# Performance work log

Hardware: AMD Instinct MI355X
Metric: run time of the kernel (lower is better)

## Reference

```python
import jax, jax.numpy as jnp
import numpy as np

EPS = 1e-5  # BatchNorm eps (eval mode, running_mean=0, running_var=1)

def bn(z, gamma, beta):
    s = gamma / jnp.sqrt(1.0 + EPS)
    return z * s[None, :, None, None] + beta[None, :, None, None]

def conv1d(x, w, b, pad):
    # x: (N,C,L), w: (O,C,K)
    y = jax.lax.conv_general_dilated(x, w, (1,), [(pad, pad)],
                                     dimension_numbers=('NCH', 'OIH', 'NCH'))
    return y + b[None, :, None]

def setup_inputs():
    key = jax.random.key(0)
    N, C, T, V = 128, 64, 128, 25
    S, H = 3, 8
    ig = C // 4   # gcn q/k embedding channels
    ih = C // H   # per-head channels
    ks = iter(jax.random.split(key, 40))
    rn = lambda shape, s=0.05: jax.random.normal(next(ks), shape, jnp.float32) * s
    inp = {}
    inp['x'] = jax.random.normal(next(ks), (N, C, T, V), jnp.float32)
    inp['A'] = jnp.stack([jnp.eye(V, dtype=jnp.float32)] * S) + jax.random.uniform(next(ks), (S, V, V), jnp.float32) * 0.05
    inp['alpha'] = jnp.float32(0.1)
    inp['Wq'] = rn((S, ig, C)); inp['bq'] = rn((S, ig))
    inp['Wk'] = rn((S, ig, C)); inp['bk'] = rn((S, ig))
    inp['Wf'] = rn((S, C, C)); inp['bf'] = rn((S, C))
    inp['g_gamma'] = jnp.ones((C,), jnp.float32); inp['g_beta'] = jnp.zeros((C,), jnp.float32)
    inp['W_sa'] = rn((1, C, V)); inp['b_sa'] = rn((1,))
    inp['W_ta'] = rn((1, C, 9)); inp['b_ta'] = rn((1,))
    inp['W_fc1'] = rn((C // 2, C)); inp['b_fc1'] = rn((C // 2,))
    inp['W_fc2'] = rn((C, C // 2)); inp['b_fc2'] = rn((C,))
    inp['pos_emb'] = rn((1, T, C * V), 0.02)
    inp['Wq_h'] = rn((H, ih, C)); inp['bq_h'] = rn((H, ih))
    inp['Wk_h'] = rn((H, ih, C)); inp['bk_h'] = rn((H, ih))
    inp['Wv_h'] = rn((H, ih, C)); inp['bv_h'] = rn((H, ih))
    inp['W_ffn'] = rn((C, C)); inp['b_ffn'] = rn((C,))
    inp['m_gamma'] = jnp.ones((C,), jnp.float32); inp['m_beta'] = jnp.zeros((C,), jnp.float32)
    return inp

def reference(x, A, alpha, Wq, bq, Wk, bk, Wf, bf, g_gamma, g_beta,
              W_sa, b_sa, W_ta, b_ta, W_fc1, b_fc1, W_fc2, b_fc2,
              pos_emb, Wq_h, bq_h, Wk_h, bk_h, Wv_h, bv_h,
              W_ffn, b_ffn, m_gamma, m_beta):
    N, C, T, V = x.shape
    S, ig = Wq.shape[0], Wq.shape[1]
    # ---------- unit_gcn_qkv (adaptive graph conv) ----------
    q = jnp.einsum('sic,nctv->nsitv', Wq, x) + bq[None, :, :, None, None]
    k = jnp.einsum('sic,nctv->nsitv', Wk, x) + bk[None, :, :, None, None]
    qf = q.transpose(0, 1, 4, 2, 3).reshape(N, S, V, ig * T)   # (N,S,V,ig*T)
    kf = k.reshape(N, S, ig * T, V)                            # (N,S,ig*T,V)
    att = jnp.einsum('nsvd,nsdw->nsvw', qf, kf) / jnp.float32(ig * T)
    att = jax.nn.softmax(att, axis=-2)                         # Softmax(dim=-2)
    Aad = A[None] + att * alpha                                # (N,S,V,V)
    xf = x.reshape(N, C * T, V)
    agg = jnp.einsum('ndv,nsvw->nsdw', xf, Aad).reshape(N, S, C, T, V)
    y = jnp.einsum('soc,nsctv->notv', Wf, agg) + bf.sum(0)[None, :, None, None]
    y = bn(y, g_gamma, g_beta) + x                             # down = identity (in==out)
    y = jax.nn.relu(y)
    # spatial / temporal / channel attention gates (MS-AAGCN style)
    se = y.mean(axis=2)                                        # (N,C,V)
    sa = jax.nn.sigmoid(conv1d(se, W_sa, b_sa, (V - 1) // 2))  # (N,1,V)
    y = y * sa[:, :, None, :] + y
    se = y.mean(axis=3)                                        # (N,C,T)
    ta = jax.nn.sigmoid(conv1d(se, W_ta, b_ta, 4))             # (N,1,T)
    y = y * ta[:, :, :, None] + y
    se = y.mean(axis=(2, 3))                                   # (N,C)
    ca = jax.nn.sigmoid(jax.nn.relu(se @ W_fc1.T + b_fc1) @ W_fc2.T + b_fc2)
    y = y * ca[:, :, None, None] + y
    # ---------- Multi-Head causal Temporal Attention ----------
    pe = pos_emb.reshape(1, T, C, V).transpose(0, 2, 1, 3)     # 'n t (d v)' -> 'n d t v'
    xa = y + pe
    H, ih = Wq_h.shape[0], Wq_h.shape[1]
    d = ih * V
    qh = (jnp.einsum('hoc,nctv->nhtov', Wq_h, xa) + bq_h[None, :, None, :, None]).reshape(N, H, T, d)
    kh = (jnp.einsum('hoc,nctv->nhtov', Wk_h, xa) + bk_h[None, :, None, :, None]).reshape(N, H, T, d)
    vh = (jnp.einsum('hoc,nctv->nhtov', Wv_h, xa) + bv_h[None, :, None, :, None]).reshape(N, H, T, d)
    scores = jnp.einsum('nhtd,nhsd->nhts', qh, kh) / jnp.sqrt(jnp.float32(d))
    causal = jnp.tril(jnp.ones((T, T), bool))
    scores = jnp.where(causal[None, None], scores, jnp.float32(-1e9))
    p = jax.nn.softmax(scores, axis=-1)
    oh = jnp.einsum('nhts,nhsd->nhtd', p, vh)
    # concat heads along emb dim, reinterpret '(d v)' -> channels-major layout
    z = oh.reshape(N, H, T, ih, V).transpose(0, 1, 3, 2, 4).reshape(N, C, T, V)
    z = bn(z, m_gamma, m_beta) + xa
    z = jax.nn.relu(jnp.einsum('oc,nctv->notv', W_ffn, z) + b_ffn[None, :, None, None]) + xa
    z = bn(z, m_gamma, m_beta)
    # ---------- unit residual ----------
    return jax.nn.relu(z + x)
```

## Files before the change

### kernel.cpp

```cpp
#include <hip/hip_runtime.h>
#include <hip/hip_bf16.h>

#define N_ 128
#define C_ 64
#define T_ 128
#define V_ 25
#define S_ 3
#define IG 16
#define IH 8
#define H_ 8
#define D_ 200
#define CV 1600
#define TV 3200
#define EPSB 1e-5f
#define NCHUNK 16

typedef __attribute__((ext_vector_type(8))) short short8v;
typedef __attribute__((ext_vector_type(4))) float f32x4;
#define MFMA16 __builtin_amdgcn_mfma_f32_16x16x32_bf16
#define ZIDX(r,c) ((r)*72 + ((c) ^ ((((r)>>3)&7)<<3)))

__device__ __forceinline__ float sigm(float x){ return 1.f/(1.f+expf(-x)); }
__device__ __forceinline__ float b2f(__hip_bfloat16 b){ return __bfloat162float(b); }
__device__ __forceinline__ __hip_bfloat16 f2b(float f){ return __float2bfloat16(f); }
__device__ __forceinline__ float ubl(unsigned int u){ return __uint_as_float(u<<16); }
__device__ __forceinline__ float ubh(unsigned int u){ return __uint_as_float(u & 0xffff0000u); }
__device__ __forceinline__ float sh2f(short s){ return __uint_as_float(((unsigned int)(unsigned short)s)<<16); }
__device__ __forceinline__ unsigned short f2bu(float f){
  unsigned int u = __float_as_uint(f);
  u += 0x7fff + ((u>>16)&1);
  return (unsigned short)(u>>16);
}
__device__ __forceinline__ unsigned long long pk4bf(f32x4 v){
  unsigned long long a = f2bu(v[0]);
  unsigned long long b = f2bu(v[1]);
  unsigned long long c = f2bu(v[2]);
  unsigned long long d = f2bu(v[3]);
  return a | (b<<16) | (c<<32) | (d<<48);
}

__global__ __launch_bounds__(256) void k_prep(
    const float* __restrict__ Wq, const float* __restrict__ Wk,
    const float* __restrict__ Wf,
    const float* __restrict__ Wq_h, const float* __restrict__ Wk_h,
    const float* __restrict__ Wv_h, const float* __restrict__ W_ffn,
    short* __restrict__ wqb, short* __restrict__ wkb, short* __restrict__ Wfb,
    short* __restrict__ w3b, short* __restrict__ Wffnb)
{
  const int i = blockIdx.x*256 + threadIdx.x;
  if (i < 3072){ wqb[i]=(short)f2bu(Wq[i]); wkb[i]=(short)f2bu(Wk[i]); }
  if (i < 12288) Wfb[i]=(short)f2bu(Wf[i]);
  if (i < 4096){
    w3b[i]      =(short)f2bu(Wq_h[i]);
    w3b[4096+i] =(short)f2bu(Wk_h[i]);
    w3b[8192+i] =(short)f2bu(Wv_h[i]);
    Wffnb[i]    =(short)f2bu(W_ffn[i]);
  }
}

__global__ __launch_bounds__(256) void k_gcn_att1(
    const float* __restrict__ x,
    const short* __restrict__ wqb, const float* __restrict__ bq,
    const short* __restrict__ wkb, const float* __restrict__ bk,
    float* __restrict__ attg)
{
  const int tc = blockIdx.x, n = blockIdx.y;
  const int tid = threadIdx.x;
  const int wv = tid>>6, l = tid&63, lc = l&15, lk = l>>4;
  __shared__ __align__(16) short xtb[4*32*72];
  __shared__ __align__(16) char QB[3*32*256];
  __shared__ __align__(16) char KB[3*32*256];
  __shared__ float bql[48], bkl[48];
  short8v aqf[3][2], akf[3][2];
  #pragma unroll
  for (int s=0;s<3;++s){
    #pragma unroll
    for (int ks=0;ks<2;++ks){
      aqf[s][ks] = *(const short8v*)(wqb + (s*16+lc)*64 + ks*32 + lk*8);
      akf[s][ks] = *(const short8v*)(wkb + (s*16+lc)*64 + ks*32 + lk*8);
    }
  }
  if (tid<48){ bql[tid]=bq[tid]; bkl[tid]=bk[tid]; }
  for (int i=tid;i<4*7*72;i+=256){
    int tl=i/(7*72), r=i%(7*72);
    xtb[(tl*32+25)*72 + r] = 0;
  }
  const float* xn = x + (size_t)n*C_*TV;
  #pragma unroll
  for (int tg=0; tg<2; ++tg){
    if (tg) __syncthreads();
    {
      const int base = tc*200 + tg*100;
      float4 xb[7];
      #pragma unroll
      for (int k=0;k<7;++k){
        int i = tid + k*256;
        if (i<1600){ int c=i/25,a=i%25; xb[k] = *(const float4*)(xn + (size_t)c*TV + base + a*4); }
      }
      #pragma unroll
      for (int k=0;k<7;++k){
        int i = tid + k*256;
        if (i<1600){
          int c=i/25,a=i%25;
          float xv[4]={xb[k].x,xb[k].y,xb[k].z,xb[k].w};
          #pragma unroll
          for (int j=0;j<4;++j){
            int tv=a*4+j, tl=tv/25, v=tv-tl*25;
            xtb[(tl*32+v)*72 + c] = (short)f2bu(xv[j]);
          }
        }
      }
    }
    __syncthreads();
    const int tcol = (tg*4+wv)*32;
    const int sw = (lc&7)<<4;
    #pragma unroll
    for (int s=0;s<3;++s){
      f32x4 z={0.f,0.f,0.f,0.f};
      f32x4 aq0=z,aq1=z,ak0=z,ak1=z;
      #pragma unroll
      for (int ks=0;ks<2;++ks){
        short8v b0 = *(const short8v*)(xtb + (wv*32+lc)*72 + ks*32 + lk*8);
        short8v b1 = *(const short8v*)(xtb + (wv*32+16+lc)*72 + ks*32 + lk*8);
        aq0 = MFMA16(aqf[s][ks], b0, aq0,0,0,0);
        aq1 = MFMA16(aqf[s][ks], b1, aq1,0,0,0);
        ak0 = MFMA16(akf[s][ks], b0, ak0,0,0,0);
        ak1 = MFMA16(akf[s][ks], b1, ak1,0,0,0);
      }
      f32x4 q0,q1,k0,k1;
      #pragma unroll
      for (int r=0;r<4;++r){
        float bqv=bql[s*16+lk*4+r], bkv=bkl[s*16+lk*4+r];
        q0[r]=aq0[r]+bqv; q1[r]=aq1[r]+bqv;
        k0[r]=ak0[r]+bkv; k1[r]=ak1[r]+bkv;
      }
      char* QBs = QB + s*8192;
      char* KBs = KB + s*8192;
      *(unsigned long long*)(QBs + ((lc*256      + tcol + lk*8) ^ sw)) = pk4bf(q0);
      *(unsigned long long*)(QBs + (((16+lc)*256 + tcol + lk*8) ^ sw)) = pk4bf(q1);
      *(unsigned long long*)(KBs + ((lc*256      + tcol + lk*8) ^ sw)) = pk4bf(k0);
      *(unsigned long long*)(KBs + (((16+lc)*256 + tcol + lk*8) ^ sw)) = pk4bf(k1);
    }
  }
  __syncthreads();
  const int mt = wv>>1, nt = wv&1;
  const int sw = (lc&7)<<4;
  #pragma unroll
  for (int s=0;s<3;++s){
    const char* QBs = QB + s*8192;
    const char* KBs = KB + s*8192;
    f32x4 acc = {0.f,0.f,0.f,0.f};
    #pragma unroll
    for (int ks=0;ks<4;++ks){
      short8v a = *(const short8v*)(QBs + (((mt*16+lc)*256 + ks*64 + lk*16) ^ sw));
      short8v b = *(const short8v*)(KBs + (((nt*16+lc)*256 + ks*64 + lk*16) ^ sw));
      acc = MFMA16(a,b,acc,0,0,0);
    }
    float* Ao = attg + ((size_t)tc*(N_*S_) + n*S_ + s)*(V_*V_);
    #pragma unroll
    for (int reg=0;reg<4;++reg){
      int v = mt*16 + lk*4 + reg, w = nt*16 + lc;
      if (v<V_ && w<V_) Ao[v*V_+w] = acc[reg];
    }
  }
}

__global__ __launch_bounds__(256) void k_gcn_att2(
    const float* __restrict__ attg, const float* __restrict__ A,
    const float* __restrict__ alphap, short* __restrict__ AsTg)
{
  const int ns = blockIdx.x, s = ns % S_, tid = threadIdx.x;
  __shared__ float att[V_*V_];
  short* dst = AsTg + (size_t)ns*1280;
  for (int i=tid;i<1280;i+=256) dst[i]=0;
  for (int i=tid;i<V_*V_;i+=256){
    float acc=0.f;
    #pragma unroll
    for (int tcc=0;tcc<NCHUNK;++tcc) acc += attg[((size_t)tcc*(N_*S_) + ns)*(V_*V_) + i];
    att[i]=acc;
  }
  __syncthreads();
  if (tid<V_){
    const int w=tid; const float inv=1.f/(IG*T_);
    float mx=-1e30f;
    for (int v=0;v<V_;++v) mx=fmaxf(mx, att[v*V_+w]*inv);
    float sum=0.f;
    for (int v=0;v<V_;++v){ float e=expf(att[v*V_+w]*inv-mx); att[v*V_+w]=e; sum+=e; }
    float rs=1.f/sum;
    for (int v=0;v<V_;++v) att[v*V_+w]*=rs;
  }
  __syncthreads();
  const float alpha=alphap[0];
  for (int i=tid;i<V_*V_;i+=256){
    int v=i/25, w=i%25;
    dst[w*40+v] = (short)f2bu(A[s*625+i] + alpha*att[i]);
  }
}

__global__ __launch_bounds__(256) void k_gcn_y(
    const float* __restrict__ x, const short* __restrict__ AsTg,
    const short* __restrict__ Wfb, const float* __restrict__ bfp,
    const float* __restrict__ g_gamma, const float* __restrict__ g_beta,
    __hip_bfloat16* __restrict__ y1)
{
  const int tc=blockIdx.x, n=blockIdx.y, tid=threadIdx.x;
  const int wv=tid>>6, l=tid&63, lc=l&15, lk=l>>4;
  __shared__ __align__(16) short xtb[64*136];
  __shared__ __align__(16) short AsT[3*32*40];
  __shared__ __align__(16) short aggT[112*200];
  const float* xn = x + (size_t)n*C_*TV;
  const int tv0 = tc*100;
  float4 xbuf[7];
  #pragma unroll
  for (int k=0;k<7;++k){
    int i = tid + k*256;
    if (i < 1600){
      int c=i/25, a=i%25;
      xbuf[k] = *(const float4*)(xn + (size_t)c*TV + tv0 + a*4);
    }
  }
  #pragma unroll
  for (int k=0;k<7;++k){
    int i = tid + k*256;
    if (i < 1600){
      int c=i/25, a=i%25, tv4=a*4;
      float xv[4] = {xbuf[k].x, xbuf[k].y, xbuf[k].z, xbuf[k].w};
      #pragma unroll
      for (int j=0;j<4;++j){
        int tv=tv4+j, t=tv/25, v=tv-t*25;
        xtb[c*136 + t*32 + v] = (short)f2bu(xv[j]);
      }
    }
  }
  for (int i=tid;i<64*28;i+=256){ int c=i/28, r=i%28; xtb[c*136 + (r/7)*32 + 25 + (r%7)] = 0; }
  {
    const short* As_g = AsTg + (size_t)n*3840;
    for (int i=tid;i<480;i+=256)
      *(short8v*)(AsT + i*8) = *(const short8v*)(As_g + i*8);
  }
  for (int i=tid;i<12*200;i+=256) aggT[100*200+i]=0;
  __syncthreads();
  {
    const int t = wv;
    for (int s=0;s<S_;++s){
      short8v b0 = *(const short8v*)(AsT + (s*32+lc)*40 + lk*8);
      short8v b1 = *(const short8v*)(AsT + (s*32+16+lc)*40 + lk*8);
      #pragma unroll
      for (int mt=0;mt<4;++mt){
        short8v a = *(const short8v*)(xtb + (mt*16+lc)*136 + t*32 + lk*8);
        f32x4 z={0.f,0.f,0.f,0.f};
        f32x4 acc0 = MFMA16(a,b0,z,0,0,0);
        f32x4 acc1 = MFMA16(a,b1,z,0,0,0);
        *(unsigned long long*)(aggT + (t*25+lc)*200 + s*64 + mt*16 + lk*4) = pk4bf(acc0);
        if (lc<9)
          *(unsigned long long*)(aggT + (t*25+16+lc)*200 + s*64 + mt*16 + lk*4) = pk4bf(acc1);
      }
    }
  }
  short8v af[6];
  #pragma unroll
  for (int ks=0;ks<6;++ks){
    const int s = ks>>1, c0 = (ks&1)*32 + lk*8;
    af[ks] = *(const short8v*)(Wfb + (size_t)(s*C_ + wv*16+lc)*C_ + c0);
  }
  __syncthreads();
  f32x4 acc[7];
  #pragma unroll
  for (int dt=0;dt<7;++dt) acc[dt]=(f32x4){0.f,0.f,0.f,0.f};
  #pragma unroll
  for (int dt=0;dt<7;++dt){
    #pragma unroll
    for (int ks=0;ks<6;++ks){
      short8v b = *(const short8v*)(aggT + (dt*16+lc)*200 + ks*32 + lk*8);
      acc[dt] = MFMA16(af[ks], b, acc[dt],0,0,0);
    }
  }
  const float invs = rsqrtf(1.f+EPSB);
  __hip_bfloat16* yo = y1 + (size_t)n*C_*TV;
  #pragma unroll
  for (int reg=0;reg<4;++reg){
    const int o = wv*16 + lk*4 + reg;
    const float bsum = bfp[o]+bfp[C_+o]+bfp[2*C_+o];
    const float gs = g_gamma[o]*invs, gb = g_beta[o];
    #pragma unroll
    for (int dt=0;dt<7;++dt){
      const int tv = dt*16 + lc;
      if (tv < 100){
        const int t = tv/25, v = tv - t*25;
        float xres = sh2f(xtb[o*136 + t*32 + v]);
        float val = (acc[dt][reg]+bsum)*gs + gb + xres;
        yo[(size_t)o*TV + tv0 + tv] = f2b(fmaxf(val,0.f));
      }
    }
  }
}

__global__ __launch_bounds__(256) void k_seT(const __hip_bfloat16* __restrict__ y1,
    float* __restrict__ seT)
{
  const int c=blockIdx.x, n=blockIdx.y, tid=threadIdx.x;
  const int v = tid&31, g = tid>>5;
  __shared__ float red[8][33];
  const __hip_bfloat16* yp = y1 + ((size_t)n*C_+c)*T_*V_;
  float s=0.f;
  if (v < V_){
    #pragma unroll 4
    for (int j=0;j<16;++j){
      int t = g + j*8;
      s += b2f(yp[t*V_+v]);
    }
  }
  red[g][v]=s;
  __syncthreads();
  if (tid < V_){
    float tot=0.f;
    #pragma unroll
    for (int g2=0;g2<8;++g2) tot += red[g2][tid];
    seT[((size_t)n*C_+c)*V_+tid]=tot*(1.f/T_);
  }
}

__global__ __launch_bounds__(256) void k_sa(const float* __restrict__ seT,
    const float* __restrict__ W_sa, const float* __restrict__ b_sa,
    float* __restrict__ sa)
{
  const int n=blockIdx.x, tid=threadIdx.x;
  __shared__ float sel[CV];
  __shared__ float wsl[CV];
  __shared__ float part[8][32];
  const float* se = seT + (size_t)n*C_*V_;
  for (int i=tid;i<CV;i+=256){ sel[i]=se[i]; wsl[i]=W_sa[i]; }
  __syncthreads();
  if (tid < 200){
    const int v = tid%25, cg = tid/25;
    float acc=0.f;
    for (int c=cg*8;c<cg*8+8;++c){
      #pragma unroll
      for (int k=0;k<V_;++k){
        int vv=v+k-12;
        if (vv>=0&&vv<V_) acc += sel[c*V_+vv]*wsl[c*V_+k];
      }
    }
    part[cg][v]=acc;
  }
  __syncthreads();
  if (tid<V_){
    float acc=b_sa[0];
    #pragma unroll
    for (int g=0;g<8;++g) acc+=part[g][tid];
    sa[n*V_+tid]=sigm(acc);
  }
}

__global__ __launch_bounds__(256) void k_seV(const __hip_bfloat16* __restrict__ y1,
    const float* __restrict__ sa, float* __restrict__ seV)
{
  const int c=blockIdx.x, n=blockIdx.y, tid=threadIdx.x;
  const int v = tid&31, g = tid>>5;
  __shared__ float sal[32];
  if (tid<32) sal[tid] = (tid<V_)? 1.f+sa[n*V_+tid] : 0.f;
  __syncthreads();
  const __hip_bfloat16* yp = y1 + ((size_t)n*C_+c)*T_*V_;
  float* svo = seV + ((size_t)n*C_+c)*T_;
  const float sv_ = sal[v];
  for (int j=0;j<16;++j){
    int t = g*16 + j;
    float val = (v<V_)? b2f(yp[t*V_+v])*sv_ : 0.f;
    #pragma unroll
    for (int off=16;off;off>>=1) val += __shfl_xor(val, off);
    if (v==0) svo[t]=val*(1.f/V_);
  }
}

__global__ __launch_bounds__(256) void k_ta_ca(const float* __restrict__ seV,
    const float* __restrict__ W_ta, const float* __restrict__ b_ta,
    const float* __restrict__ W_fc1, const float* __restrict__ b_fc1,
    const float* __restrict__ W_fc2, const float* __restrict__ b_fc2,
    float* __restrict__ ta, float* __restrict__ ca)
{
  const int n=blockIdx.x, tid=threadIdx.x;
  __shared__ float svl[C_*T_];
  __shared__ float wtl[C_*9];
  __shared__ float w1l[32*C_];
  __shared__ float w2l[C_*32];
  __shared__ float tal[T_];
  __shared__ float part2[2][T_];
  __shared__ float part4[C_][4];
  __shared__ float scls[C_];
  __shared__ float h1[32];
  const float* sv = seV + (size_t)n*C_*T_;
  for (int i=tid;i<C_*T_;i+=256) svl[i]=sv[i];
  for (int i=tid;i<C_*9;i+=256) wtl[i]=W_ta[i];
  for (int i=tid;i<32*C_;i+=256){ w1l[i]=W_fc1[i]; w2l[i]=W_fc2[i]; }
  __syncthreads();
  {
    const int t = tid & 127, half = tid >> 7;
    float acc = 0.f;
    for (int c=half*32; c<half*32+32; ++c){
      #pragma unroll
      for (int k=0;k<9;++k){
        int tt=t+k-4;
        if (tt>=0&&tt<T_) acc += svl[c*T_+tt]*wtl[c*9+k];
      }
    }
    part2[half][t]=acc;
  }
  __syncthreads();
  if (tid<T_){
    float s_=sigm(part2[0][tid]+part2[1][tid]+b_ta[0]);
    tal[tid]=s_; ta[n*T_+tid]=s_;
  }
  __syncthreads();
  {
    const int c = tid>>2, q = tid&3;
    float acc=0.f;
    for (int t=q*32;t<q*32+32;++t) acc += svl[c*T_+t]*(1.f+tal[t]);
    part4[c][q]=acc;
  }
  __syncthreads();
  if (tid<C_) scls[tid]=(part4[tid][0]+part4[tid][1]+part4[tid][2]+part4[tid][3])*(1.f/T_);
  __syncthreads();
  if (tid<32){
    float acc=b_fc1[tid];
    for (int c=0;c<C_;++c) acc += scls[c]*w1l[tid*C_+c];
    h1[tid]=fmaxf(acc,0.f);
  }
  __syncthreads();
  if (tid<C_){
    float acc=b_fc2[tid];
    for (int j=0;j<32;++j) acc += h1[j]*w2l[tid*32+j];
    ca[n*C_+tid]=sigm(acc);
  }
}

__global__ __launch_bounds__(256) void k_xa_qkv(
    const __hip_bfloat16* __restrict__ y1, const float* __restrict__ pos_emb,
    const float* __restrict__ sa, const float* __restrict__ ta, const float* __restrict__ ca,
    const short* __restrict__ w3b, const float* __restrict__ bq_h,
    const float* __restrict__ bk_h, const float* __restrict__ bv_h,
    __hip_bfloat16* __restrict__ xa, __hip_bfloat16* __restrict__ qb,
    __hip_bfloat16* __restrict__ kb, __hip_bfloat16* __restrict__ vb)
{
  const int tc=blockIdx.x, n=blockIdx.y, tid=threadIdx.x;
  const int wv=tid>>6, l=tid&63, lc=l&15, lk=l>>4;
  __shared__ __align__(16) short w3[192*72];
  __shared__ __align__(16) short xalT[4][32*72];
  __shared__ float bl[192];
  __shared__ float sal[32], cal[64], tgs[4];
  const int tv0 = tc*100;
  const __hip_bfloat16* y1n = y1 + (size_t)n*C_*TV;
  __hip_bfloat16* xan = xa + (size_t)n*C_*TV;
  uint2 ybuf[7];
  #pragma unroll
  for (int k=0;k<7;++k){
    int i = tid + k*256;
    if (i < 1600){
      int c=i/25, a=i%25;
      ybuf[k] = *(const uint2*)(y1n + (size_t)c*TV + tv0 + a*4);
    }
  }
  for (int i=tid;i<1536;i+=256){
    int mu=i>>3, j=i&7;
    *(short8v*)(w3 + mu*72 + j*8) = *(const short8v*)(w3b + mu*64 + j*8);
  }
  if (tid<192){
    int which=tid/C_, ho=tid%C_;
    bl[tid] = (which==0?bq_h:(which==1?bk_h:bv_h))[ho];
  }
  if (tid<32) sal[tid] = (tid<V_)? 1.f+sa[n*V_+tid] : 0.f;
  if (tid>=32 && tid<96) cal[tid-32] = 1.f+ca[n*C_+tid-32];
  if (tid>=96 && tid<100) tgs[tid-96] = 1.f+ta[n*T_+tc*4+(tid-96)];
  for (int i=tid;i<4*7*72;i+=256){
    int tl=i/(7*72), r=i%(7*72);
    xalT[tl][25*72 + r] = 0;
  }
  __syncthreads();
  #pragma unroll
  for (int k=0;k<7;++k){
    int i = tid + k*256;
    if (i < 1600){
      int c=i/25, a=i%25, tv4=a*4;
      unsigned int u0=ybuf[k].x, u1=ybuf[k].y;
      float yv[4] = {ubl(u0),ubh(u0),ubl(u1),ubh(u1)};
      const float calc = cal[c];
      unsigned long long pack = 0ull;
      #pragma unroll
      for (int j=0;j<4;++j){
        int tv=tv4+j, tl=tv/25, v=tv-tl*25;
        float val = yv[j]*sal[v]*tgs[tl]*calc + pos_emb[(size_t)(tc*4+tl)*CV + c*V_ + v];
        unsigned short b = f2bu(val);
        pack |= (unsigned long long)b << (16*j);
        xalT[tl][v*72 + c] = (short)b;
      }
      *(unsigned long long*)(xan + (size_t)c*TV + tv0 + tv4) = pack;
    }
  }
  __syncthreads();
  const int t = tc*4 + wv;
  short8v bf_[2][2];
  #pragma unroll
  for (int ks=0;ks<2;++ks){
    bf_[ks][0] = *(const short8v*)(&xalT[wv][lc*72      + ks*32 + lk*8]);
    bf_[ks][1] = *(const short8v*)(&xalT[wv][(16+lc)*72 + ks*32 + lk*8]);
  }
  #pragma unroll
  for (int mt=0;mt<12;++mt){
    f32x4 acc0 = {0.f,0.f,0.f,0.f}, acc1 = {0.f,0.f,0.f,0.f};
    #pragma unroll
    for (int ks=0;ks<2;++ks){
      short8v a = *(const short8v*)(w3 + (mt*16+lc)*72 + ks*32 + lk*8);
      acc0 = MFMA16(a, bf_[ks][0], acc0,0,0,0);
      acc1 = MFMA16(a, bf_[ks][1], acc1,0,0,0);
    }
    #pragma unroll
    for (int reg=0;reg<4;++reg){
      const int mu = mt*16 + lk*4 + reg;
      const int which = mt>>2;
      const int ho = mu & 63, h = ho>>3, o = ho&7;
      __hip_bfloat16* dst = (which==0?qb:(which==1?kb:vb))
                            + (((size_t)n*H_+h)*T_+t)*D_ + o*V_;
      const float bb = bl[mu];
      dst[lc] = f2b(acc0[reg]+bb);
      if (lc < 9) dst[16+lc] = f2b(acc1[reg]+bb);
    }
  }
}

__global__ __launch_bounds__(256) void k_attn(
    const __hip_bfloat16* __restrict__ qb, const __hip_bfloat16* __restrict__ kb,
    const __hip_bfloat16* __restrict__ vb, __hip_bfloat16* __restrict__ oh)
{
  const int bx = blockIdx.x;
  const int hh = blockIdx.y;
  const int n  = blockIdx.z;
  const int nh = n*H_ + hh;
  const int tid = threadIdx.x;
  const int wv = tid>>6, l = tid&63;
  const int lc = l&15, lg = l>>4;
  __shared__ __align__(16) char KlB[32*512];
  __shared__ __align__(16) short VT[208*40];
  __shared__ __align__(16) short Pl[64*40];
  const __hip_bfloat16* qg_ = qb + (size_t)nh*T_*D_;
  const __hip_bfloat16* kg_ = kb + (size_t)nh*T_*D_;
  const __hip_bfloat16* vg_ = vb + (size_t)nh*T_*D_;
  __hip_bfloat16* ohn = oh + (size_t)n*C_*TV;
  const float scale = 0.0707106781f;

  for (int i=tid;i<32*12;i+=256){
    int key=i/12, j=i%12;
    *(unsigned int*)(KlB + ((key*512 + 400 + j*4) ^ ((key&7)<<4))) = 0u;
  }
  for (int i=tid;i<8*40;i+=256) VT[200*40 + i] = 0;

  const int qrow = bx*64 + wv*16 + lc;
  short8v qf[7];
  {
    const short8v* qs8 = (const short8v*)(qg_ + (size_t)qrow*D_);
    #pragma unroll
    for (int ks=0;ks<7;++ks) qf[ks] = qs8[ks*4 + lg];
  }
  f32x4 oacc[13];
  #pragma unroll
  for (int i=0;i<13;++i) oacc[i] = (f32x4){0.f,0.f,0.f,0.f};
  float m[4], lsm[4];
  #pragma unroll
  for (int r=0;r<4;++r){ m[r]=-1e30f; lsm[r]=0.f; }

  const int ntiles = (bx==0)? 2 : 4;
  short8v kreg[4], vreg[4];
  {
    const short8v* ks8 = (const short8v*)(kg_);
    const short8v* vs8 = (const short8v*)(vg_);
    #pragma unroll
    for (int k=0;k<4;++k){
      int i = tid + k*256;
      if (i<800){
        kreg[k] = ks8[i];
        vreg[k] = vs8[(i&31)*25 + (i>>5)];
      }
    }
  }
  for (int kt=0; kt<ntiles; ++kt){
    const int j0 = kt*32;
    #pragma unroll
    for (int k=0;k<4;++k){
      int i = tid + k*256;
      if (i<800){
        int row=i/25, w=i%25;
        *(short8v*)(KlB + ((row*512 + w*16) ^ ((row&7)<<4))) = kreg[k];
        int rowv=i&31, w4=i>>5;
        short8v u = vreg[k];
        #pragma unroll
        for (int j=0;j<8;++j) VT[(w4*8+j)*40 + rowv] = u[j];
      }
    }
    __syncthreads();
    if (kt+1 < ntiles){
      const short8v* ks8 = (const short8v*)(kg_ + (size_t)(kt+1)*32*D_);
      const short8v* vs8 = (const short8v*)(vg_ + (size_t)(kt+1)*32*D_);
      #pragma unroll
      for (int k=0;k<4;++k){
        int i = tid + k*256;
        if (i<800){
          kreg[k] = ks8[i];
          vreg[k] = vs8[(i&31)*25 + (i>>5)];
        }
      }
    }
    const bool active = (j0 <= bx*64 + wv*16 + 15);
    if (active){
      f32x4 s0 = {0.f,0.f,0.f,0.f}, s1 = {0.f,0.f,0.f,0.f};
      #pragma unroll
      for (int ks=0;ks<7;++ks){
        short8v b0 = *(const short8v*)(KlB + ((lc*512      + ks*64 + lg*16) ^ ((lc&7)<<4)));
        short8v b1 = *(const short8v*)(KlB + (((16+lc)*512 + ks*64 + lg*16) ^ ((lc&7)<<4)));
        s0 = MFMA16(qf[ks], b0, s0,0,0,0);
        s1 = MFMA16(qf[ks], b1, s1,0,0,0);
      }
      float fr[4];
      #pragma unroll
      for (int r=0;r<4;++r){
        const int qg = bx*64 + wv*16 + lg*4 + r;
        float v0 = (j0+lc    <= qg) ? s0[r]*scale : -1e30f;
        float v1 = (j0+16+lc <= qg) ? s1[r]*scale : -1e30f;
        float mx = fmaxf(v0,v1);
        #pragma unroll
        for (int off=1;off<16;off<<=1) mx = fmaxf(mx, __shfl_xor(mx, off));
        float mn = fmaxf(m[r], mx);
        fr[r] = __expf(m[r]-mn);
        float p0 = __expf(v0-mn), p1 = __expf(v1-mn);
        float ts = p0+p1;
        #pragma unroll
        for (int off=1;off<16;off<<=1) ts += __shfl_xor(ts, off);
        lsm[r] = lsm[r]*fr[r] + ts;
        m[r] = mn;
        Pl[(wv*16 + lg*4 + r)*40 + lc]      = (short)f2bu(p0);
        Pl[(wv*16 + lg*4 + r)*40 + 16 + lc] = (short)f2bu(p1);
      }
      #pragma unroll
      for (int dt=0;dt<13;++dt){
        #pragma unroll
        for (int r=0;r<4;++r) oacc[dt][r] *= fr[r];
      }
      short8v pa = *(const short8v*)(Pl + (wv*16+lc)*40 + lg*8);
      #pragma unroll
      for (int dt=0;dt<13;++dt){
        short8v b = *(const short8v*)(VT + (dt*16+lc)*40 + lg*8);
        oacc[dt] = MFMA16(pa, b, oacc[dt],0,0,0);
      }
    }
    __syncthreads();
  }
  float rl[4];
  #pragma unroll
  for (int r=0;r<4;++r) rl[r] = 1.f/lsm[r];
  #pragma unroll
  for (int dt=0;dt<13;++dt){
    const int d = dt*16 + lc;
    if (d < D_){
      const int oi = d/25, v = d - oi*25;
      const int c = hh*IH + oi;
      #pragma unroll
      for (int r=0;r<4;++r){
        const int q = bx*64 + wv*16 + lg*4 + r;
        ohn[(size_t)c*TV + q*V_ + v] = f2b(oacc[dt][r]*rl[r]);
      }
    }
  }
}

__global__ __launch_bounds__(256) void k_out(
    const __hip_bfloat16* __restrict__ oh, const __hip_bfloat16* __restrict__ xa,
    const float* __restrict__ x, const short* __restrict__ Wffnb,
    const float* __restrict__ b_ffn, const float* __restrict__ m_gamma,
    const float* __restrict__ m_beta, float* __restrict__ out)
{
  const int tc = blockIdx.x, n = blockIdx.y, tid = threadIdx.x;
  const int wv = tid>>6, l = tid&63, lc = l&15, lg = l>>4;
  __shared__ __align__(16) short zT[208*72];
  __shared__ float bn_s[64], bn_b[64], bff[64];
  const float invs = rsqrtf(1.f+EPSB);
  if (tid<64){ bn_s[tid]=m_gamma[tid]*invs; bn_b[tid]=m_beta[tid]; bff[tid]=b_ffn[tid]; }
  for (int i=tid;i<8*72;i+=256) zT[200*72+i]=0;
  const int tv0 = tc*200;
  const __hip_bfloat16* xan = xa + (size_t)n*C_*TV;
  const __hip_bfloat16* ohn = oh + (size_t)n*C_*TV;
  uint4 xbuf[7], obuf[7];
  #pragma unroll
  for (int k=0;k<7;++k){
    int i = tid + k*256;
    if (i < 1600){
      int c=i/25, a=i%25;
      xbuf[k] = *(const uint4*)(xan + (size_t)c*TV + tv0 + a*8);
      obuf[k] = *(const uint4*)(ohn + (size_t)c*TV + tv0 + a*8);
    }
  }
  __syncthreads();
  #pragma unroll
  for (int k=0;k<7;++k){
    int i = tid + k*256;
    if (i < 1600){
      int c=i/25, a=i%25, tv8=a*8;
      const float s_=bn_s[c], b_=bn_b[c];
      const unsigned int* xu = (const unsigned int*)&xbuf[k];
      const unsigned int* ou = (const unsigned int*)&obuf[k];
      #pragma unroll
      for (int j=0;j<4;++j){
        zT[ZIDX(tv8+2*j,   c)] = (short)f2bu(s_*ubl(ou[j]) + b_ + ubl(xu[j]));
        zT[ZIDX(tv8+2*j+1, c)] = (short)f2bu(s_*ubh(ou[j]) + b_ + ubh(xu[j]));
      }
    }
  }
  __syncthreads();
  short8v af0 = *(const short8v*)(Wffnb + (wv*16+lc)*64 + lg*8);
  short8v af1 = *(const short8v*)(Wffnb + (wv*16+lc)*64 + 32 + lg*8);
  f32x4 acc[13];
  #pragma unroll
  for (int dt=0;dt<13;++dt) acc[dt] = (f32x4){0.f,0.f,0.f,0.f};
  #pragma unroll
  for (int dt=0;dt<13;++dt){
    short8v b0 = *(const short8v*)(zT + ZIDX(dt*16+lc, lg*8));
    short8v b1 = *(const short8v*)(zT + ZIDX(dt*16+lc, 32+lg*8));
    acc[dt] = MFMA16(af0, b0, acc[dt],0,0,0);
    acc[dt] = MFMA16(af1, b1, acc[dt],0,0,0);
  }
  __syncthreads();
  #pragma unroll
  for (int dt=0;dt<13;++dt){
    const int tv = dt*16 + lc;
    if (tv < 200){
      #pragma unroll
      for (int reg=0;reg<4;++reg){
        const int o = wv*16 + lg*4 + reg;
        zT[ZIDX(tv, o)] = (short)f2bu(acc[dt][reg]);
      }
    }
  }
  __syncthreads();
  const float* xn = x + (size_t)n*C_*TV;
  float* outn = out + (size_t)n*C_*TV;
  #pragma unroll
  for (int k=0;k<7;++k){
    int i = tid + k*256;
    if (i < 1600){
      const int c=i/25, a=i%25, tv8=a*8;
      const unsigned int* xu = (const unsigned int*)&xbuf[k];
      const float s_=bn_s[c], b_=bn_b[c], bf_=bff[c];
      float4 xf0 = *(const float4*)(xn + (size_t)c*TV + tv0 + tv8);
      float4 xf1 = *(const float4*)(xn + (size_t)c*TV + tv0 + tv8 + 4);
      float xf[8] = {xf0.x,xf0.y,xf0.z,xf0.w,xf1.x,xf1.y,xf1.z,xf1.w};
      float res[8];
      #pragma unroll
      for (int j=0;j<4;++j){
        float xal = ubl(xu[j]), xah = ubh(xu[j]);
        float f0 = sh2f(zT[ZIDX(tv8+2*j,   c)]);
        float f1 = sh2f(zT[ZIDX(tv8+2*j+1, c)]);
        res[2*j]   = fmaxf(s_*(fmaxf(f0+bf_,0.f)+xal)+b_ + xf[2*j],   0.f);
        res[2*j+1] = fmaxf(s_*(fmaxf(f1+bf_,0.f)+xah)+b_ + xf[2*j+1], 0.f);
      }
      float4 o0 = {res[0],res[1],res[2],res[3]};
      float4 o1 = {res[4],res[5],res[6],res[7]};
      *(float4*)(outn + (size_t)c*TV + tv0 + tv8)     = o0;
      *(float4*)(outn + (size_t)c*TV + tv0 + tv8 + 4) = o1;
    }
  }
}

extern "C" void kernel_launch(void* const* d_in, const int* in_sizes, int n_in,
                              void* d_out, int out_size, void* d_ws, size_t ws_size,
                              hipStream_t stream) {
  const float* x      = (const float*)d_in[0];
  const float* A      = (const float*)d_in[1];
  const float* alphap = (const float*)d_in[2];
  const float* Wq     = (const float*)d_in[3];
  const float* bq     = (const float*)d_in[4];
  const float* Wk     = (const float*)d_in[5];
  const float* bk     = (const float*)d_in[6];
  const float* Wf     = (const float*)d_in[7];
  const float* bfp    = (const float*)d_in[8];
  const float* g_gamma= (const float*)d_in[9];
  const float* g_beta = (const float*)d_in[10];
  const float* W_sa   = (const float*)d_in[11];
  const float* b_sa   = (const float*)d_in[12];
  const float* W_ta   = (const float*)d_in[13];
  const float* b_ta   = (const float*)d_in[14];
  const float* W_fc1  = (const float*)d_in[15];
  const float* b_fc1  = (const float*)d_in[16];
  const float* W_fc2  = (const float*)d_in[17];
  const float* b_fc2  = (const float*)d_in[18];
  const float* pos_emb= (const float*)d_in[19];
  const float* Wq_h   = (const float*)d_in[20];
  const float* bq_h   = (const float*)d_in[21];
  const float* Wk_h   = (const float*)d_in[22];
  const float* bk_h   = (const float*)d_in[23];
  const float* Wv_h   = (const float*)d_in[24];
  const float* bv_h   = (const float*)d_in[25];
  const float* W_ffn  = (const float*)d_in[26];
  const float* b_ffn  = (const float*)d_in[27];
  const float* m_gamma= (const float*)d_in[28];
  const float* m_beta = (const float*)d_in[29];
  float* out = (float*)d_out;

  float* ws   = (float*)d_ws;
  float* seT  = ws;
  float* seV  = seT + 204800;
  float* sa   = seV + 1048576;
  float* ta   = sa  + 3200;
  float* ca   = ta  + 16384;
  short* wsh  = (short*)(ca + 8192);
  short* AsTg = wsh;
  short* wqb  = AsTg + 491520;
  short* wkb  = wqb + 3072;
  short* Wfb  = wkb + 3072;
  short* w3b  = Wfb + 12288;
  short* Wffnb= w3b + 12288;
  __hip_bfloat16* y1 = (__hip_bfloat16*)(Wffnb + 4096);
  __hip_bfloat16* xa = y1 + (size_t)26214400;
  __hip_bfloat16* qb = xa + (size_t)26214400;
  __hip_bfloat16* kb = qb + (size_t)26214400;
  __hip_bfloat16* vb = kb + (size_t)26214400;
  __hip_bfloat16* oh = y1;
  float* attg = (float*)y1;

  k_prep<<<48, 256, 0, stream>>>(Wq, Wk, Wf, Wq_h, Wk_h, Wv_h, W_ffn,
                                 wqb, wkb, Wfb, w3b, Wffnb);
  k_gcn_att1<<<dim3(16, N_), 256, 0, stream>>>(x, wqb, bq, wkb, bk, attg);
  k_gcn_att2<<<N_*S_, 256, 0, stream>>>(attg, A, alphap, AsTg);
  k_gcn_y<<<dim3(T_/4, N_), 256, 0, stream>>>(x, AsTg, Wfb, bfp, g_gamma, g_beta, y1);
  k_seT<<<dim3(C_, N_), 256, 0, stream>>>(y1, seT);
  k_sa<<<N_, 256, 0, stream>>>(seT, W_sa, b_sa, sa);
  k_seV<<<dim3(C_, N_), 256, 0, stream>>>(y1, sa, seV);
  k_ta_ca<<<N_, 256, 0, stream>>>(seV, W_ta, b_ta, W_fc1, b_fc1, W_fc2, b_fc2, ta, ca);
  k_xa_qkv<<<dim3(T_/4, N_), 256, 0, stream>>>(y1, pos_emb, sa, ta, ca,
      w3b, bq_h, bk_h, bv_h, xa, qb, kb, vb);
  k_attn<<<dim3(2, H_, N_), 256, 0, stream>>>(qb, kb, vb, oh);
  k_out<<<dim3(T_/8, N_), 256, 0, stream>>>(oh, xa, x, Wffnb, b_ffn, m_gamma, m_beta, out);
}
```

Measured before the change: 431.7 us.

## Recompute xa in output kernel, stage QKV in LDS for coalesced stores

Drops the materialised xa tensor. The output kernel now recomputes xa from y1, pos_emb and the sa/ta/ca gates, which removes one full bf16 write and one read of the activation. The QKV projection results are staged in LDS and written with coalesced 32-bit stores instead of scattered 16-bit ones, and the weight matrix is read directly from global memory instead of being copied to LDS. The cost is extra pos_emb reads and arithmetic in k_out, and oh moves to a separate buffer so y1 stays readable.

Measured after the change: 498.1 us. 1.15x slower.

```diff
diff --git a/kernel.cpp b/kernel.cpp
--- a/kernel.cpp
+++ b/kernel.cpp
@@ -438,18 +438,17 @@
     const float* __restrict__ sa, const float* __restrict__ ta, const float* __restrict__ ca,
     const short* __restrict__ w3b, const float* __restrict__ bq_h,
     const float* __restrict__ bk_h, const float* __restrict__ bv_h,
-    __hip_bfloat16* __restrict__ xa, __hip_bfloat16* __restrict__ qb,
-    __hip_bfloat16* __restrict__ kb, __hip_bfloat16* __restrict__ vb)
+    __hip_bfloat16* __restrict__ qb, __hip_bfloat16* __restrict__ kb,
+    __hip_bfloat16* __restrict__ vb)
 {
   const int tc=blockIdx.x, n=blockIdx.y, tid=threadIdx.x;
   const int wv=tid>>6, l=tid&63, lc=l&15, lk=l>>4;
-  __shared__ __align__(16) short w3[192*72];
   __shared__ __align__(16) short xalT[4][32*72];
+  __shared__ __align__(16) short qkvl[3*8*4*200];
   __shared__ float bl[192];
   __shared__ float sal[32], cal[64], tgs[4];
   const int tv0 = tc*100;
   const __hip_bfloat16* y1n = y1 + (size_t)n*C_*TV;
-  __hip_bfloat16* xan = xa + (size_t)n*C_*TV;
   uint2 ybuf[7];
   #pragma unroll
   for (int k=0;k<7;++k){
@@ -458,10 +457,6 @@
       int c=i/25, a=i%25;
       ybuf[k] = *(const uint2*)(y1n + (size_t)c*TV + tv0 + a*4);
     }
-  }
-  for (int i=tid;i<1536;i+=256){
-    int mu=i>>3, j=i&7;
-    *(short8v*)(w3 + mu*72 + j*8) = *(const short8v*)(w3b + mu*64 + j*8);
   }
   if (tid<192){
     int which=tid/C_, ho=tid%C_;
@@ -483,20 +478,15 @@
       unsigned int u0=ybuf[k].x, u1=ybuf[k].y;
       float yv[4] = {ubl(u0),ubh(u0),ubl(u1),ubh(u1)};
       const float calc = cal[c];
-      unsigned long long pack = 0ull;
       #pragma unroll
       for (int j=0;j<4;++j){
         int tv=tv4+j, tl=tv/25, v=tv-tl*25;
         float val = yv[j]*sal[v]*tgs[tl]*calc + pos_emb[(size_t)(tc*4+tl)*CV + c*V_ + v];
-        unsigned short b = f2bu(val);
-        pack |= (unsigned long long)b << (16*j);
-        xalT[tl][v*72 + c] = (short)b;
-      }
-      *(unsigned long long*)(xan + (size_t)c*TV + tv0 + tv4) = pack;
-    }
-  }
-  __syncthreads();
-  const int t = tc*4 + wv;
+        xalT[tl][v*72 + c] = (short)f2bu(val);
+      }
+    }
+  }
+  __syncthreads();
   short8v bf_[2][2];
   #pragma unroll
   for (int ks=0;ks<2;++ks){
@@ -508,7 +498,7 @@
     f32x4 acc0 = {0.f,0.f,0.f,0.f}, acc1 = {0.f,0.f,0.f,0.f};
     #pragma unroll
     for (int ks=0;ks<2;++ks){
-      short8v a = *(const short8v*)(w3 + (mt*16+lc)*72 + ks*32 + lk*8);
+      short8v a = *(const short8v*)(w3b + (mt*16+lc)*64 + ks*32 + lk*8);
       acc0 = MFMA16(a, bf_[ks][0], acc0,0,0,0);
       acc1 = MFMA16(a, bf_[ks][1], acc1,0,0,0);
     }
@@ -517,12 +507,18 @@
       const int mu = mt*16 + lk*4 + reg;
       const int which = mt>>2;
       const int ho = mu & 63, h = ho>>3, o = ho&7;
-      __hip_bfloat16* dst = (which==0?qb:(which==1?kb:vb))
-                            + (((size_t)n*H_+h)*T_+t)*D_ + o*V_;
+      const int base = ((which*8+h)*4 + wv)*200 + o*V_;
       const float bb = bl[mu];
-      dst[lc] = f2b(acc0[reg]+bb);
-      if (lc < 9) dst[16+lc] = f2b(acc1[reg]+bb);
-    }
+      qkvl[base + lc] = (short)f2bu(acc0[reg]+bb);
+      if (lc < 9) qkvl[base + 16 + lc] = (short)f2bu(acc1[reg]+bb);
+    }
+  }
+  __syncthreads();
+  const unsigned int* ql = (const unsigned int*)qkvl;
+  for (int i=tid;i<9600;i+=256){
+    int which = i/3200, r=i%3200, h=r/400, r2=r%400, tl=r2/100, d2=r2%100;
+    __hip_bfloat16* dst = (which==0?qb:(which==1?kb:vb));
+    *(unsigned int*)(dst + ((((size_t)n*H_+h)*T_ + tc*4+tl)*D_ + d2*2)) = ql[i];
   }
 }
 
@@ -670,7 +666,9 @@
 }
 
 __global__ __launch_bounds__(256) void k_out(
-    const __hip_bfloat16* __restrict__ oh, const __hip_bfloat16* __restrict__ xa,
+    const __hip_bfloat16* __restrict__ oh, const __hip_bfloat16* __restrict__ y1,
+    const float* __restrict__ pos_emb,
+    const float* __restrict__ sa, const float* __restrict__ ta, const float* __restrict__ ca,
     const float* __restrict__ x, const short* __restrict__ Wffnb,
     const float* __restrict__ b_ffn, const float* __restrict__ m_gamma,
     const float* __restrict__ m_beta, float* __restrict__ out)
@@ -679,35 +677,48 @@
   const int wv = tid>>6, l = tid&63, lc = l&15, lg = l>>4;
   __shared__ __align__(16) short zT[208*72];
   __shared__ float bn_s[64], bn_b[64], bff[64];
+  __shared__ float sal[32], cal[64], tgs8[8];
   const float invs = rsqrtf(1.f+EPSB);
   if (tid<64){ bn_s[tid]=m_gamma[tid]*invs; bn_b[tid]=m_beta[tid]; bff[tid]=b_ffn[tid]; }
+  if (tid>=64 && tid<96) sal[tid-64] = (tid-64<V_)? 1.f+sa[n*V_+tid-64] : 0.f;
+  if (tid>=96 && tid<160) cal[tid-96] = 1.f+ca[n*C_+tid-96];
+  if (tid>=160 && tid<168) tgs8[tid-160] = 1.f+ta[n*T_+tc*8+(tid-160)];
   for (int i=tid;i<8*72;i+=256) zT[200*72+i]=0;
   const int tv0 = tc*200;
-  const __hip_bfloat16* xan = xa + (size_t)n*C_*TV;
+  const __hip_bfloat16* y1n = y1 + (size_t)n*C_*TV;
   const __hip_bfloat16* ohn = oh + (size_t)n*C_*TV;
-  uint4 xbuf[7], obuf[7];
+  uint4 ybuf[7], obuf[7];
   #pragma unroll
   for (int k=0;k<7;++k){
     int i = tid + k*256;
     if (i < 1600){
       int c=i/25, a=i%25;
-      xbuf[k] = *(const uint4*)(xan + (size_t)c*TV + tv0 + a*8);
+      ybuf[k] = *(const uint4*)(y1n + (size_t)c*TV + tv0 + a*8);
       obuf[k] = *(const uint4*)(ohn + (size_t)c*TV + tv0 + a*8);
     }
   }
   __syncthreads();
+  unsigned int xabuf[7][4];
   #pragma unroll
   for (int k=0;k<7;++k){
     int i = tid + k*256;
     if (i < 1600){
       int c=i/25, a=i%25, tv8=a*8;
-      const float s_=bn_s[c], b_=bn_b[c];
-      const unsigned int* xu = (const unsigned int*)&xbuf[k];
+      const float s_=bn_s[c], b_=bn_b[c], calc=cal[c];
+      const unsigned int* yu = (const unsigned int*)&ybuf[k];
       const unsigned int* ou = (const unsigned int*)&obuf[k];
+      const float* pe = pos_emb + (size_t)tc*8*CV + c*V_;
       #pragma unroll
       for (int j=0;j<4;++j){
-        zT[ZIDX(tv8+2*j,   c)] = (short)f2bu(s_*ubl(ou[j]) + b_ + ubl(xu[j]));
-        zT[ZIDX(tv8+2*j+1, c)] = (short)f2bu(s_*ubh(ou[j]) + b_ + ubh(xu[j]));
+        int tva=tv8+2*j, tvb=tva+1;
+        int ta_=tva/25, va=tva-ta_*25;
+        int tb_=tvb/25, vb_=tvb-tb_*25;
+        float xav = ubl(yu[j])*sal[va]*tgs8[ta_]*calc + pe[(size_t)ta_*CV + va];
+        float xbv = ubh(yu[j])*sal[vb_]*tgs8[tb_]*calc + pe[(size_t)tb_*CV + vb_];
+        unsigned int pk = (unsigned int)f2bu(xav) | ((unsigned int)f2bu(xbv)<<16);
+        xabuf[k][j] = pk;
+        zT[ZIDX(tva, c)] = (short)f2bu(s_*ubl(ou[j]) + b_ + xav);
+        zT[ZIDX(tvb, c)] = (short)f2bu(s_*ubh(ou[j]) + b_ + xbv);
       }
     }
   }
@@ -744,7 +755,6 @@
     int i = tid + k*256;
     if (i < 1600){
       const int c=i/25, a=i%25, tv8=a*8;
-      const unsigned int* xu = (const unsigned int*)&xbuf[k];
       const float s_=bn_s[c], b_=bn_b[c], bf_=bff[c];
       float4 xf0 = *(const float4*)(xn + (size_t)c*TV + tv0 + tv8);
       float4 xf1 = *(const float4*)(xn + (size_t)c*TV + tv0 + tv8 + 4);
@@ -752,7 +762,7 @@
       float res[8];
       #pragma unroll
       for (int j=0;j<4;++j){
-        float xal = ubl(xu[j]), xah = ubh(xu[j]);
+        float xal = ubl(xabuf[k][j]), xah = ubh(xabuf[k][j]);
         float f0 = sh2f(zT[ZIDX(tv8+2*j,   c)]);
         float f1 = sh2f(zT[ZIDX(tv8+2*j+1, c)]);
         res[2*j]   = fmaxf(s_*(fmaxf(f0+bf_,0.f)+xal)+b_ + xf[2*j],   0.f);
@@ -815,11 +825,10 @@
   short* w3b  = Wfb + 12288;
   short* Wffnb= w3b + 12288;
   __hip_bfloat16* y1 = (__hip_bfloat16*)(Wffnb + 4096);
-  __hip_bfloat16* xa = y1 + (size_t)26214400;
-  __hip_bfloat16* qb = xa + (size_t)26214400;
+  __hip_bfloat16* qb = y1 + (size_t)26214400;
   __hip_bfloat16* kb = qb + (size_t)26214400;
   __hip_bfloat16* vb = kb + (size_t)26214400;
-  __hip_bfloat16* oh = y1;
+  __hip_bfloat16* oh = vb + (size_t)26214400;
   float* attg = (float*)y1;
 
   k_prep<<<48, 256, 0, stream>>>(Wq, Wk, Wf, Wq_h, Wk_h, Wv_h, W_ffn,
@@ -832,7 +841,8 @@
   k_seV<<<dim3(C_, N_), 256, 0, stream>>>(y1, sa, seV);
   k_ta_ca<<<N_, 256, 0, stream>>>(seV, W_ta, b_ta, W_fc1, b_fc1, W_fc2, b_fc2, ta, ca);
   k_xa_qkv<<<dim3(T_/4, N_), 256, 0, stream>>>(y1, pos_emb, sa, ta, ca,
-      w3b, bq_h, bk_h, bv_h, xa, qb, kb, vb);
+      w3b, bq_h, bk_h, bv_h, qb, kb, vb);
   k_attn<<<dim3(2, H_, N_), 256, 0, stream>>>(qb, kb, vb, oh);
-  k_out<<<dim3(T_/8, N_), 256, 0, stream>>>(oh, xa, x, Wffnb, b_ffn, m_gamma, m_beta, out);
-}
+  k_out<<<dim3(T_/8, N_), 256, 0, stream>>>(oh, y1, pos_emb, sa, ta, ca,
+      x, Wffnb, b_ffn, m_gamma, m_beta, out);
+}
```
